# Optimization experiments

Measured on AMD Instinct MI355X. Metric: run time of the kernel, lower is better.

Reference implementation:

```python
import jax, jax.numpy as jnp
import numpy as np

LN_EPS = 1e-5  # torch nn.LayerNorm default


def layernorm(x, g, b):
    mu = jnp.mean(x, axis=-1, keepdims=True)
    var = jnp.var(x, axis=-1, keepdims=True)
    return (x - mu) * jax.lax.rsqrt(var + LN_EPS) * g + b


def setup_inputs() -> dict:
    key = jax.random.key(0)
    ks = jax.random.split(key, 12)
    B, N, Dn, Dm, E, L = 4, 20000, 64, 128, 160000, 2
    inp = {}
    inp["node_feat"] = jax.random.normal(ks[0], (B, N, Dn), jnp.float32)
    inp["in_W"] = jax.random.normal(ks[1], (Dn, Dm), jnp.float32) * 0.1
    inp["in_b"] = jnp.zeros((Dm,), jnp.float32)
    inp["node_W"] = jax.random.normal(ks[2], (L, 3, Dm, Dm), jnp.float32) * 0.05
    inp["node_b"] = jnp.zeros((L, 3, Dm), jnp.float32)
    inp["edge_W"] = jax.random.normal(ks[3], (L, 2, 16, Dm), jnp.float32) * 0.1
    inp["edge_b"] = jnp.zeros((L, 2, Dm), jnp.float32)
    inp["ln_g"] = jnp.ones((L, Dm), jnp.float32)
    inp["ln_b"] = jnp.zeros((L, Dm), jnp.float32)
    inp["ea0"] = jax.random.normal(ks[4], (E, 16), jnp.float32)
    inp["ea1"] = jax.random.normal(ks[5], (E, 16), jnp.float32)
    inp["ei0"] = jax.random.randint(ks[6], (2, E), 0, N)
    inp["ei1"] = jax.random.randint(ks[7], (2, E), 0, N)
    inp["ei2"] = jax.random.randint(ks[8], (2, E), 0, N)
    return inp


def reference(node_feat, in_W, in_b, node_W, node_b, edge_W, edge_b, ln_g, ln_b,
              ea0, ea1, ei0, ei1, ei2):
    # input projection: [B,N,Dn] -> [B,N,Dm]
    H = node_feat @ in_W + in_b
    edge_idx = [ei0, ei1, ei2]
    edge_attr = [ea0, ea1, None]  # relation 2 has edge_attr_dims == 0 (Identity/skip)
    n_layers = node_W.shape[0]
    for l in range(n_layers):
        agg = jnp.zeros_like(H)
        for r in range(3):
            src, dst = edge_idx[r][0], edge_idx[r][1]
            # gather src nodes per batch then per-relation linear: [B,E,Dm]
            msg = H[:, src] @ node_W[l, r] + node_b[l, r]
            if edge_attr[r] is not None:
                # edge attrs shared across batch -> broadcast add
                msg = msg + (edge_attr[r] @ edge_W[l, r] + edge_b[l, r])[None]
            # scatter-add messages to dst nodes, batched
            agg = agg.at[:, dst].add(msg)
        H = layernorm(H + jax.nn.relu(agg), ln_g[l], ln_b[l])
    return H
```

## Files before the change

kernel.cpp:

```cpp
#include <hip/hip_runtime.h>


#define NNODES 20000
#define NB     4
#define BROWS  (NB * NNODES)
#define DN     64
#define DM     128
#define NE     160000
#define CAP    64
#define LN_EPS 1e-5f
#define KE     448
#define LDW    88

typedef __attribute__((ext_vector_type(8))) short bf16x8;
typedef __attribute__((ext_vector_type(4))) float f32x4;

__device__ inline float bf2f(unsigned short u) {
    union { unsigned int i; float f; } x; x.i = ((unsigned int)u) << 16; return x.f;
}
__device__ inline unsigned short f2bf(float f) {
    union { float f; unsigned int i; } x; x.f = f;
    unsigned int r = x.i + 0x7FFFu + ((x.i >> 16) & 1u);
    return (unsigned short)(r >> 16);
}

__global__ void k_scatter(const int* __restrict__ ei0, const int* __restrict__ ei1,
                          const int* __restrict__ ei2, int* __restrict__ cursor,
                          int* __restrict__ srcs, int* __restrict__ eids) {
    int tid = blockIdx.x * blockDim.x + threadIdx.x;
    if (tid >= 3 * NE) return;
    int r = tid / NE, e = tid - r * NE;
    const int* ei = (r == 0) ? ei0 : ((r == 1) ? ei1 : ei2);
    int src = ei[e], dst = ei[NE + e];
    int p = atomicAdd(&cursor[r * NNODES + dst], 1);
    if (p < CAP) {
        srcs[(r * NNODES + dst) * CAP + p] = src;
        if (r < 2) eids[(r * NNODES + dst) * CAP + p] = e;
    }
}

__global__ __launch_bounds__(256) void k_sgather(const int* __restrict__ deg,
                                                 const int* __restrict__ eids,
                                                 const float* __restrict__ ea0,
                                                 const float* __restrict__ ea1,
                                                 float* __restrict__ S) {
    int task = blockIdx.x * 4 + (threadIdx.x >> 6);
    int r = task / NNODES;
    const float* ea = r ? ea1 : ea0;
    int lane = threadIdx.x & 63;
    int k = lane & 15, sub = lane >> 4;
    int dg = deg[task]; if (dg > CAP) dg = CAP;
    const int* bk = eids + (size_t)task * CAP;
    float acc = 0.f;
    for (int j = sub; j < dg; j += 4) {
        int e = bk[j];
        acc += ea[e * 16 + k];
    }
    acc += __shfl_xor(acc, 16, 64);
    acc += __shfl_xor(acc, 32, 64);
    if (lane < 16) S[(size_t)task * 16 + k] = acc;
}

__global__ __launch_bounds__(256) void k_wprep(const float* __restrict__ nW,
                                               const float* __restrict__ nb,
                                               const float* __restrict__ eW,
                                               const float* __restrict__ eb,
                                               const float* __restrict__ inW,
                                               unsigned short* __restrict__ Wt,
                                               unsigned short* __restrict__ Wp) {
    int lin = blockIdx.x * 256 + threadIdx.x;
    if (lin < 2 * 128 * KE) {
        int l = lin / (128 * KE);
        int rem = lin - l * 128 * KE;
        int n = rem / KE, k = rem - n * KE;
        float v;
        if (k < 384) {
            int r = k >> 7, kk = k & 127;
            v = nW[(((size_t)(l * 3 + r) * 128) + kk) * 128 + n];
        } else {
            int e = k - 384;
            if (e < 3) {
                v = nb[(l * 3 + e) * DM + n];
                if (e < 2) v += eb[(l * 2 + e) * DM + n];
            } else if (e < 35) {
                int r2 = (e - 3) >> 4, j = (e - 3) & 15;
                v = eW[((size_t)((l * 2 + r2) * 16 + j)) * DM + n];
            } else v = 0.f;
        }
        Wt[lin] = f2bf(v);
    } else {
        int i = lin - 2 * 128 * KE;
        int n = i >> 6, k = i & 63;
        Wp[n * 64 + k] = f2bf(inW[(size_t)k * DM + n]);
    }
}

__global__ __launch_bounds__(256) void k_proj(const float* __restrict__ X,
                                              const unsigned short* __restrict__ Wp,
                                              const float* __restrict__ bias,
                                              unsigned short* __restrict__ HB) {
    __shared__ __align__(16) unsigned short As[64][LDW];
    __shared__ __align__(16) unsigned short Bs[128][LDW];
    int t = threadIdx.x;
    int m0 = blockIdx.x * 64;
#pragma unroll
    for (int i = 0; i < 4; ++i) {
        int lin = t + 256 * i;
        int row = lin >> 4, seg = lin & 15;
        float4 v = *(const float4*)(X + (size_t)(m0 + row) * DN + seg * 4);
        ushort4 h; h.x = f2bf(v.x); h.y = f2bf(v.y); h.z = f2bf(v.z); h.w = f2bf(v.w);
        *(ushort4*)&As[row][seg * 4] = h;
    }
#pragma unroll
    for (int i = 0; i < 4; ++i) {
        int lin = t + 256 * i;
        int row = lin >> 3, seg = lin & 7;
        *(uint4*)&Bs[row][seg * 8] = *(const uint4*)(Wp + (size_t)row * 64 + seg * 8);
    }
    __syncthreads();
    int w = t >> 6, lane = t & 63;
    int q = lane >> 4, lm = lane & 15;
    f32x4 acc[8];
#pragma unroll
    for (int ct = 0; ct < 8; ++ct) acc[ct] = (f32x4){0.f, 0.f, 0.f, 0.f};
#pragma unroll
    for (int kt = 0; kt < 2; ++kt) {
        bf16x8 a = *(const bf16x8*)&As[w * 16 + lm][kt * 32 + q * 8];
#pragma unroll
        for (int ct = 0; ct < 8; ++ct) {
            bf16x8 bf = *(const bf16x8*)&Bs[ct * 16 + lm][kt * 32 + q * 8];
            acc[ct] = __builtin_amdgcn_mfma_f32_16x16x32_bf16(a, bf, acc[ct], 0, 0, 0);
        }
    }
#pragma unroll
    for (int reg = 0; reg < 4; ++reg) {
        int row = m0 + w * 16 + q * 4 + reg;
#pragma unroll
        for (int ct = 0; ct < 8; ++ct) {
            int col = ct * 16 + lm;
            HB[(size_t)row * DM + col] = f2bf(acc[ct][reg] + bias[col]);
        }
    }
}

__global__ __launch_bounds__(256) void k_spmm(const unsigned short* __restrict__ HB,
                                              const int* __restrict__ deg,
                                              const int* __restrict__ srcs,
                                              const float* __restrict__ S,
                                              unsigned short* __restrict__ G) {
    int blk = blockIdx.x;
    int s = blk & 7;
    int bb = s >> 1;
    int idx = ((blk >> 3) << 1) + (s & 1);
    int n0 = idx * 16;
    int g = threadIdx.x >> 4, lane = threadIdx.x & 15;
    int n = n0 + g;
    int c8 = lane * 8;
    const unsigned short* Hb = HB + (size_t)bb * NNODES * DM;
    size_t rowbase = ((size_t)(bb * NNODES + n)) * KE;
    int dt[3];
#pragma unroll
    for (int r = 0; r < 3; ++r) {
        dt[r] = deg[r * NNODES + n];
        int dg = dt[r] > CAP ? CAP : dt[r];
        const int* bk = srcs + (size_t)(r * NNODES + n) * CAP;
        float a[8];
#pragma unroll
        for (int j = 0; j < 8; ++j) a[j] = 0.f;
        int j = 0;
        for (; j + 3 < dg; j += 4) {
            int4 s4 = *(const int4*)&bk[j];
            ushort4 u0 = *(const ushort4*)(Hb + (size_t)s4.x * DM + c8);
            ushort4 u1 = *(const ushort4*)(Hb + (size_t)s4.x * DM + c8 + 4);
            ushort4 v0 = *(const ushort4*)(Hb + (size_t)s4.y * DM + c8);
            ushort4 v1 = *(const ushort4*)(Hb + (size_t)s4.y * DM + c8 + 4);
            ushort4 w0 = *(const ushort4*)(Hb + (size_t)s4.z * DM + c8);
            ushort4 w1 = *(const ushort4*)(Hb + (size_t)s4.z * DM + c8 + 4);
            ushort4 x0 = *(const ushort4*)(Hb + (size_t)s4.w * DM + c8);
            ushort4 x1 = *(const ushort4*)(Hb + (size_t)s4.w * DM + c8 + 4);
            a[0] += bf2f(u0.x) + bf2f(v0.x) + bf2f(w0.x) + bf2f(x0.x);
            a[1] += bf2f(u0.y) + bf2f(v0.y) + bf2f(w0.y) + bf2f(x0.y);
            a[2] += bf2f(u0.z) + bf2f(v0.z) + bf2f(w0.z) + bf2f(x0.z);
            a[3] += bf2f(u0.w) + bf2f(v0.w) + bf2f(w0.w) + bf2f(x0.w);
            a[4] += bf2f(u1.x) + bf2f(v1.x) + bf2f(w1.x) + bf2f(x1.x);
            a[5] += bf2f(u1.y) + bf2f(v1.y) + bf2f(w1.y) + bf2f(x1.y);
            a[6] += bf2f(u1.z) + bf2f(v1.z) + bf2f(w1.z) + bf2f(x1.z);
            a[7] += bf2f(u1.w) + bf2f(v1.w) + bf2f(w1.w) + bf2f(x1.w);
        }
        for (; j < dg; ++j) {
            int s0 = bk[j];
            ushort4 u0 = *(const ushort4*)(Hb + (size_t)s0 * DM + c8);
            ushort4 u1 = *(const ushort4*)(Hb + (size_t)s0 * DM + c8 + 4);
            a[0] += bf2f(u0.x); a[1] += bf2f(u0.y); a[2] += bf2f(u0.z); a[3] += bf2f(u0.w);
            a[4] += bf2f(u1.x); a[5] += bf2f(u1.y); a[6] += bf2f(u1.z); a[7] += bf2f(u1.w);
        }
        ushort4 o0, o1;
        o0.x = f2bf(a[0]); o0.y = f2bf(a[1]); o0.z = f2bf(a[2]); o0.w = f2bf(a[3]);
        o1.x = f2bf(a[4]); o1.y = f2bf(a[5]); o1.z = f2bf(a[6]); o1.w = f2bf(a[7]);
        *(ushort4*)(G + rowbase + r * 128 + c8) = o0;
        *(ushort4*)(G + rowbase + r * 128 + c8 + 4) = o1;
    }
    if (lane < 8) {
        ushort4 e0, e1;
        unsigned short ev[8];
#pragma unroll
        for (int j = 0; j < 8; ++j) {
            int kk = lane * 8 + j;
            float v;
            if (kk < 3)       v = (float)dt[kk];
            else if (kk < 19) v = S[((size_t)(0 * NNODES + n)) * 16 + (kk - 3)];
            else if (kk < 35) v = S[((size_t)(1 * NNODES + n)) * 16 + (kk - 19)];
            else              v = 0.f;
            ev[j] = f2bf(v);
        }
        e0.x = ev[0]; e0.y = ev[1]; e0.z = ev[2]; e0.w = ev[3];
        e1.x = ev[4]; e1.y = ev[5]; e1.z = ev[6]; e1.w = ev[7];
        *(ushort4*)(G + rowbase + 384 + lane * 8) = e0;
        *(ushort4*)(G + rowbase + 384 + lane * 8 + 4) = e1;
    }
}

__global__ __launch_bounds__(256) void k_gemm_ln(const unsigned short* __restrict__ G,
                                                 const unsigned short* __restrict__ Wt,
                                                 unsigned short* HB,
                                                 const float* __restrict__ lng,
                                                 const float* __restrict__ lnb,
                                                 float* __restrict__ out, int write_f32) {
    __shared__ __align__(16) unsigned short Gs[64][LDW];
    __shared__ __align__(16) unsigned short Ws[128][LDW];
    int t = threadIdx.x;
    int m0 = blockIdx.x * 64;
    int w = t >> 6, lane = t & 63;
    int q = lane >> 4, lm = lane & 15;

    f32x4 acc[8];
#pragma unroll
    for (int ct = 0; ct < 8; ++ct) acc[ct] = (f32x4){0.f, 0.f, 0.f, 0.f};

    for (int kc = 0; kc < 7; ++kc) {
#pragma unroll
        for (int i = 0; i < 2; ++i) {
            int lin = t + 256 * i;
            int row = lin >> 3, seg = lin & 7;
            *(uint4*)&Gs[row][seg * 8] =
                *(const uint4*)(G + (size_t)(m0 + row) * KE + kc * 64 + seg * 8);
        }
#pragma unroll
        for (int i = 0; i < 4; ++i) {
            int lin = t + 256 * i;
            int row = lin >> 3, seg = lin & 7;
            *(uint4*)&Ws[row][seg * 8] =
                *(const uint4*)(Wt + (size_t)row * KE + kc * 64 + seg * 8);
        }
        __syncthreads();
#pragma unroll
        for (int kt = 0; kt < 2; ++kt) {
            bf16x8 a = *(const bf16x8*)&Gs[w * 16 + lm][kt * 32 + q * 8];
#pragma unroll
            for (int ct = 0; ct < 8; ++ct) {
                bf16x8 bf = *(const bf16x8*)&Ws[ct * 16 + lm][kt * 32 + q * 8];
                acc[ct] = __builtin_amdgcn_mfma_f32_16x16x32_bf16(a, bf, acc[ct], 0, 0, 0);
            }
        }
        __syncthreads();
    }

    float gc[8], bc[8];
#pragma unroll
    for (int ct = 0; ct < 8; ++ct) {
        int col = ct * 16 + lm;
        gc[ct] = lng[col]; bc[ct] = lnb[col];
    }
#pragma unroll
    for (int reg = 0; reg < 4; ++reg) {
        size_t row = (size_t)m0 + w * 16 + q * 4 + reg;
        float xv[8];
        float s1 = 0.f, s2 = 0.f;
#pragma unroll
        for (int ct = 0; ct < 8; ++ct) {
            int col = ct * 16 + lm;
            float h = bf2f(HB[row * DM + col]);
            float v = h + fmaxf(acc[ct][reg], 0.f);
            xv[ct] = v; s1 += v; s2 += v * v;
        }
#pragma unroll
        for (int m = 1; m <= 8; m <<= 1) {
            s1 += __shfl_xor(s1, m, 64);
            s2 += __shfl_xor(s2, m, 64);
        }
        float mu  = s1 * (1.f / 128.f);
        float var = s2 * (1.f / 128.f) - mu * mu;
        float inv = rsqrtf(var + LN_EPS);
        if (write_f32) {
#pragma unroll
            for (int ct = 0; ct < 8; ++ct) {
                int col = ct * 16 + lm;
                out[row * DM + col] = (xv[ct] - mu) * inv * gc[ct] + bc[ct];
            }
        } else {
#pragma unroll
            for (int ct = 0; ct < 8; ++ct) {
                int col = ct * 16 + lm;
                HB[row * DM + col] = f2bf((xv[ct] - mu) * inv * gc[ct] + bc[ct]);
            }
        }
    }
}

extern "C" void kernel_launch(void* const* d_in, const int* in_sizes, int n_in,
                              void* d_out, int out_size, void* d_ws, size_t ws_size,
                              hipStream_t stream) {
    const float* node_feat = (const float*)d_in[0];
    const float* in_W   = (const float*)d_in[1];
    const float* in_b   = (const float*)d_in[2];
    const float* node_W = (const float*)d_in[3];
    const float* node_b = (const float*)d_in[4];
    const float* edge_W = (const float*)d_in[5];
    const float* edge_b = (const float*)d_in[6];
    const float* ln_g   = (const float*)d_in[7];
    const float* ln_b   = (const float*)d_in[8];
    const float* ea0    = (const float*)d_in[9];
    const float* ea1    = (const float*)d_in[10];
    const int*   ei0    = (const int*)d_in[11];
    const int*   ei1    = (const int*)d_in[12];
    const int*   ei2    = (const int*)d_in[13];
    float* out = (float*)d_out;

    char* ws = (char*)d_ws;
    size_t off = 0;
    auto alloc = [&](size_t bytes) -> void* {
        void* p = ws + off;
        off = (off + bytes + 255) & ~(size_t)255;
        return p;
    };
    unsigned short* HB     = (unsigned short*)alloc((size_t)BROWS * DM * 2);
    unsigned short* G      = (unsigned short*)alloc((size_t)BROWS * KE * 2);
    int*            cursor = (int*)alloc((size_t)3 * NNODES * 4);
    float*          S      = (float*)alloc((size_t)2 * NNODES * 16 * 4);
    int*            srcs   = (int*)alloc((size_t)3 * NNODES * CAP * 4);
    int*            eids   = (int*)alloc((size_t)2 * NNODES * CAP * 4);
    unsigned short* Wt     = (unsigned short*)alloc((size_t)2 * 128 * KE * 2);
    unsigned short* Wp     = (unsigned short*)alloc((size_t)128 * 64 * 2);

    hipMemsetAsync(cursor, 0, (size_t)3 * NNODES * 4, stream);

    k_scatter<<<(3 * NE + 255) / 256, 256, 0, stream>>>(ei0, ei1, ei2, cursor, srcs, eids);
    k_sgather<<<(2 * NNODES) / 4, 256, 0, stream>>>(cursor, eids, ea0, ea1, S);
    k_wprep<<<480, 256, 0, stream>>>(node_W, node_b, edge_W, edge_b, in_W, Wt, Wp);
    k_proj<<<BROWS / 64, 256, 0, stream>>>(node_feat, Wp, in_b, HB);

    for (int l = 0; l < 2; ++l) {
        k_spmm<<<5000, 256, 0, stream>>>(HB, cursor, srcs, S, G);
        k_gemm_ln<<<BROWS / 64, 256, 0, stream>>>(G, Wt + (size_t)l * 128 * KE, HB,
                                                  ln_g + (size_t)l * DM, ln_b + (size_t)l * DM,
                                                  out, l == 1);
    }
}
```

Measured before the change: 332.2 us.

## Prefetch gather indices, pre-scale source offsets, widen loads, double GEMM row tile

```diff
diff --git a/kernel.cpp b/kernel.cpp
--- a/kernel.cpp
+++ b/kernel.cpp
@@ -14,6 +14,8 @@
 
 typedef __attribute__((ext_vector_type(8))) short bf16x8;
 typedef __attribute__((ext_vector_type(4))) float f32x4;
+typedef __attribute__((ext_vector_type(2))) float f32x2;
+typedef __attribute__((ext_vector_type(8))) unsigned short u16x8;
 
 __device__ inline float bf2f(unsigned short u) {
     union { unsigned int i; float f; } x; x.i = ((unsigned int)u) << 16; return x.f;
@@ -22,6 +24,11 @@
     union { float f; unsigned int i; } x; x.f = f;
     unsigned int r = x.i + 0x7FFFu + ((x.i >> 16) & 1u);
     return (unsigned short)(r >> 16);
+}
+__device__ inline f32x2 bfpair(unsigned int w) {
+    union { unsigned int u; float f; } lo, hi;
+    lo.u = w << 16; hi.u = w & 0xffff0000u;
+    return (f32x2){lo.f, hi.f};
 }
 
 __global__ void k_scatter(const int* __restrict__ ei0, const int* __restrict__ ei1,
@@ -34,7 +41,7 @@
     int src = ei[e], dst = ei[NE + e];
     int p = atomicAdd(&cursor[r * NNODES + dst], 1);
     if (p < CAP) {
-        srcs[(r * NNODES + dst) * CAP + p] = src;
+        srcs[(r * NNODES + dst) * CAP + p] = src << 8;
         if (r < 2) eids[(r * NNODES + dst) * CAP + p] = e;
     }
 }
@@ -143,6 +150,34 @@
     }
 }
 
+__device__ inline void gather_rel(const char* __restrict__ HbB, unsigned c16,
+                                  const int* __restrict__ bk, int dg, int4 s4,
+                                  f32x2* a) {
+#pragma unroll
+    for (int i = 0; i < 4; ++i) a[i] = (f32x2){0.f, 0.f};
+    int j = 0;
+    while (j + 3 < dg) {
+        bool more = (j + 7 < dg);
+        int4 nxt = s4;
+        if (more) nxt = *(const int4*)(bk + j + 4);
+        uint4 u0 = *(const uint4*)(HbB + ((unsigned)s4.x + c16));
+        uint4 u1 = *(const uint4*)(HbB + ((unsigned)s4.y + c16));
+        uint4 u2 = *(const uint4*)(HbB + ((unsigned)s4.z + c16));
+        uint4 u3 = *(const uint4*)(HbB + ((unsigned)s4.w + c16));
+        a[0] += bfpair(u0.x) + bfpair(u1.x) + bfpair(u2.x) + bfpair(u3.x);
+        a[1] += bfpair(u0.y) + bfpair(u1.y) + bfpair(u2.y) + bfpair(u3.y);
+        a[2] += bfpair(u0.z) + bfpair(u1.z) + bfpair(u2.z) + bfpair(u3.z);
+        a[3] += bfpair(u0.w) + bfpair(u1.w) + bfpair(u2.w) + bfpair(u3.w);
+        j += 4;
+        s4 = nxt;
+    }
+    for (; j < dg; ++j) {
+        uint4 u = *(const uint4*)(HbB + ((unsigned)bk[j] + c16));
+        a[0] += bfpair(u.x); a[1] += bfpair(u.y);
+        a[2] += bfpair(u.z); a[3] += bfpair(u.w);
+    }
+}
+
 __global__ __launch_bounds__(256) void k_spmm(const unsigned short* __restrict__ HB,
                                               const int* __restrict__ deg,
                                               const int* __restrict__ srcs,
@@ -155,54 +190,39 @@
     int n0 = idx * 16;
     int g = threadIdx.x >> 4, lane = threadIdx.x & 15;
     int n = n0 + g;
-    int c8 = lane * 8;
-    const unsigned short* Hb = HB + (size_t)bb * NNODES * DM;
+    unsigned c16 = (unsigned)lane * 16;
+    const char* HbB = (const char*)HB + (size_t)bb * NNODES * DM * 2;
     size_t rowbase = ((size_t)(bb * NNODES + n)) * KE;
-    int dt[3];
-#pragma unroll
-    for (int r = 0; r < 3; ++r) {
-        dt[r] = deg[r * NNODES + n];
-        int dg = dt[r] > CAP ? CAP : dt[r];
-        const int* bk = srcs + (size_t)(r * NNODES + n) * CAP;
-        float a[8];
-#pragma unroll
-        for (int j = 0; j < 8; ++j) a[j] = 0.f;
-        int j = 0;
-        for (; j + 3 < dg; j += 4) {
-            int4 s4 = *(const int4*)&bk[j];
-            ushort4 u0 = *(const ushort4*)(Hb + (size_t)s4.x * DM + c8);
-            ushort4 u1 = *(const ushort4*)(Hb + (size_t)s4.x * DM + c8 + 4);
-            ushort4 v0 = *(const ushort4*)(Hb + (size_t)s4.y * DM + c8);
-            ushort4 v1 = *(const ushort4*)(Hb + (size_t)s4.y * DM + c8 + 4);
-            ushort4 w0 = *(const ushort4*)(Hb + (size_t)s4.z * DM + c8);
-            ushort4 w1 = *(const ushort4*)(Hb + (size_t)s4.z * DM + c8 + 4);
-            ushort4 x0 = *(const ushort4*)(Hb + (size_t)s4.w * DM + c8);
-            ushort4 x1 = *(const ushort4*)(Hb + (size_t)s4.w * DM + c8 + 4);
-            a[0] += bf2f(u0.x) + bf2f(v0.x) + bf2f(w0.x) + bf2f(x0.x);
-            a[1] += bf2f(u0.y) + bf2f(v0.y) + bf2f(w0.y) + bf2f(x0.y);
-            a[2] += bf2f(u0.z) + bf2f(v0.z) + bf2f(w0.z) + bf2f(x0.z);
-            a[3] += bf2f(u0.w) + bf2f(v0.w) + bf2f(w0.w) + bf2f(x0.w);
-            a[4] += bf2f(u1.x) + bf2f(v1.x) + bf2f(w1.x) + bf2f(x1.x);
-            a[5] += bf2f(u1.y) + bf2f(v1.y) + bf2f(w1.y) + bf2f(x1.y);
-            a[6] += bf2f(u1.z) + bf2f(v1.z) + bf2f(w1.z) + bf2f(x1.z);
-            a[7] += bf2f(u1.w) + bf2f(v1.w) + bf2f(w1.w) + bf2f(x1.w);
-        }
-        for (; j < dg; ++j) {
-            int s0 = bk[j];
-            ushort4 u0 = *(const ushort4*)(Hb + (size_t)s0 * DM + c8);
-            ushort4 u1 = *(const ushort4*)(Hb + (size_t)s0 * DM + c8 + 4);
-            a[0] += bf2f(u0.x); a[1] += bf2f(u0.y); a[2] += bf2f(u0.z); a[3] += bf2f(u0.w);
-            a[4] += bf2f(u1.x); a[5] += bf2f(u1.y); a[6] += bf2f(u1.z); a[7] += bf2f(u1.w);
-        }
-        ushort4 o0, o1;
-        o0.x = f2bf(a[0]); o0.y = f2bf(a[1]); o0.z = f2bf(a[2]); o0.w = f2bf(a[3]);
-        o1.x = f2bf(a[4]); o1.y = f2bf(a[5]); o1.z = f2bf(a[6]); o1.w = f2bf(a[7]);
-        *(ushort4*)(G + rowbase + r * 128 + c8) = o0;
-        *(ushort4*)(G + rowbase + r * 128 + c8 + 4) = o1;
-    }
+
+    int dt0 = deg[n], dt1 = deg[NNODES + n], dt2 = deg[2 * NNODES + n];
+    const int* bk0 = srcs + (size_t)n * CAP;
+    const int* bk1 = bk0 + (size_t)NNODES * CAP;
+    const int* bk2 = bk1 + (size_t)NNODES * CAP;
+    int4 f0 = *(const int4*)bk0;
+    int4 f1 = *(const int4*)bk1;
+    int4 f2 = *(const int4*)bk2;
+
+    f32x2 a[4];
+    u16x8 o;
+
+    gather_rel(HbB, c16, bk0, dt0 > CAP ? CAP : dt0, f0, a);
+#pragma unroll
+    for (int i = 0; i < 4; ++i) { o[2 * i] = f2bf(a[i].x); o[2 * i + 1] = f2bf(a[i].y); }
+    *(u16x8*)(G + rowbase + 0 * 128 + lane * 8) = o;
+
+    gather_rel(HbB, c16, bk1, dt1 > CAP ? CAP : dt1, f1, a);
+#pragma unroll
+    for (int i = 0; i < 4; ++i) { o[2 * i] = f2bf(a[i].x); o[2 * i + 1] = f2bf(a[i].y); }
+    *(u16x8*)(G + rowbase + 1 * 128 + lane * 8) = o;
+
+    gather_rel(HbB, c16, bk2, dt2 > CAP ? CAP : dt2, f2, a);
+#pragma unroll
+    for (int i = 0; i < 4; ++i) { o[2 * i] = f2bf(a[i].x); o[2 * i + 1] = f2bf(a[i].y); }
+    *(u16x8*)(G + rowbase + 2 * 128 + lane * 8) = o;
+
     if (lane < 8) {
-        ushort4 e0, e1;
-        unsigned short ev[8];
+        int dt[3] = {dt0, dt1, dt2};
+        u16x8 e;
 #pragma unroll
         for (int j = 0; j < 8; ++j) {
             int kk = lane * 8 + j;
@@ -211,12 +231,9 @@
             else if (kk < 19) v = S[((size_t)(0 * NNODES + n)) * 16 + (kk - 3)];
             else if (kk < 35) v = S[((size_t)(1 * NNODES + n)) * 16 + (kk - 19)];
             else              v = 0.f;
-            ev[j] = f2bf(v);
-        }
-        e0.x = ev[0]; e0.y = ev[1]; e0.z = ev[2]; e0.w = ev[3];
-        e1.x = ev[4]; e1.y = ev[5]; e1.z = ev[6]; e1.w = ev[7];
-        *(ushort4*)(G + rowbase + 384 + lane * 8) = e0;
-        *(ushort4*)(G + rowbase + 384 + lane * 8 + 4) = e1;
+            e[j] = f2bf(v);
+        }
+        *(u16x8*)(G + rowbase + 384 + lane * 8) = e;
     }
 }
 
@@ -226,20 +243,22 @@
                                                  const float* __restrict__ lng,
                                                  const float* __restrict__ lnb,
                                                  float* __restrict__ out, int write_f32) {
-    __shared__ __align__(16) unsigned short Gs[64][LDW];
+    __shared__ __align__(16) unsigned short Gs[128][LDW];
     __shared__ __align__(16) unsigned short Ws[128][LDW];
     int t = threadIdx.x;
-    int m0 = blockIdx.x * 64;
+    int m0 = blockIdx.x * 128;
     int w = t >> 6, lane = t & 63;
     int q = lane >> 4, lm = lane & 15;
 
-    f32x4 acc[8];
-#pragma unroll
-    for (int ct = 0; ct < 8; ++ct) acc[ct] = (f32x4){0.f, 0.f, 0.f, 0.f};
+    f32x4 acc[2][8];
+#pragma unroll
+    for (int af = 0; af < 2; ++af)
+#pragma unroll
+        for (int ct = 0; ct < 8; ++ct) acc[af][ct] = (f32x4){0.f, 0.f, 0.f, 0.f};
 
     for (int kc = 0; kc < 7; ++kc) {
 #pragma unroll
-        for (int i = 0; i < 2; ++i) {
+        for (int i = 0; i < 4; ++i) {
             int lin = t + 256 * i;
             int row = lin >> 3, seg = lin & 7;
             *(uint4*)&Gs[row][seg * 8] =
@@ -255,11 +274,13 @@
         __syncthreads();
 #pragma unroll
         for (int kt = 0; kt < 2; ++kt) {
-            bf16x8 a = *(const bf16x8*)&Gs[w * 16 + lm][kt * 32 + q * 8];
+            bf16x8 a0 = *(const bf16x8*)&Gs[w * 16 + lm][kt * 32 + q * 8];
+            bf16x8 a1 = *(const bf16x8*)&Gs[64 + w * 16 + lm][kt * 32 + q * 8];
 #pragma unroll
             for (int ct = 0; ct < 8; ++ct) {
                 bf16x8 bf = *(const bf16x8*)&Ws[ct * 16 + lm][kt * 32 + q * 8];
-                acc[ct] = __builtin_amdgcn_mfma_f32_16x16x32_bf16(a, bf, acc[ct], 0, 0, 0);
+                acc[0][ct] = __builtin_amdgcn_mfma_f32_16x16x32_bf16(a0, bf, acc[0][ct], 0, 0, 0);
+                acc[1][ct] = __builtin_amdgcn_mfma_f32_16x16x32_bf16(a1, bf, acc[1][ct], 0, 0, 0);
             }
         }
         __syncthreads();
@@ -272,36 +293,39 @@
         gc[ct] = lng[col]; bc[ct] = lnb[col];
     }
 #pragma unroll
-    for (int reg = 0; reg < 4; ++reg) {
-        size_t row = (size_t)m0 + w * 16 + q * 4 + reg;
-        float xv[8];
-        float s1 = 0.f, s2 = 0.f;
-#pragma unroll
-        for (int ct = 0; ct < 8; ++ct) {
-            int col = ct * 16 + lm;
-            float h = bf2f(HB[row * DM + col]);
-            float v = h + fmaxf(acc[ct][reg], 0.f);
-            xv[ct] = v; s1 += v; s2 += v * v;
-        }
-#pragma unroll
-        for (int m = 1; m <= 8; m <<= 1) {
-            s1 += __shfl_xor(s1, m, 64);
-            s2 += __shfl_xor(s2, m, 64);
-        }
-        float mu  = s1 * (1.f / 128.f);
-        float var = s2 * (1.f / 128.f) - mu * mu;
-        float inv = rsqrtf(var + LN_EPS);
-        if (write_f32) {
+    for (int af = 0; af < 2; ++af) {
+#pragma unroll
+        for (int reg = 0; reg < 4; ++reg) {
+            size_t row = (size_t)m0 + af * 64 + w * 16 + q * 4 + reg;
+            float xv[8];
+            float s1 = 0.f, s2 = 0.f;
 #pragma unroll
             for (int ct = 0; ct < 8; ++ct) {
                 int col = ct * 16 + lm;
-                out[row * DM + col] = (xv[ct] - mu) * inv * gc[ct] + bc[ct];
+                float h = bf2f(HB[row * DM + col]);
+                float v = h + fmaxf(acc[af][ct][reg], 0.f);
+                xv[ct] = v; s1 += v; s2 += v * v;
             }
-        } else {
-#pragma unroll
-            for (int ct = 0; ct < 8; ++ct) {
-                int col = ct * 16 + lm;
-                HB[row * DM + col] = f2bf((xv[ct] - mu) * inv * gc[ct] + bc[ct]);
+#pragma unroll
+            for (int m = 1; m <= 8; m <<= 1) {
+                s1 += __shfl_xor(s1, m, 64);
+                s2 += __shfl_xor(s2, m, 64);
+            }
+            float mu  = s1 * (1.f / 128.f);
+            float var = s2 * (1.f / 128.f) - mu * mu;
+            float inv = rsqrtf(var + LN_EPS);
+            if (write_f32) {
+#pragma unroll
+                for (int ct = 0; ct < 8; ++ct) {
+                    int col = ct * 16 + lm;
+                    out[row * DM + col] = (xv[ct] - mu) * inv * gc[ct] + bc[ct];
+                }
+            } else {
+#pragma unroll
+                for (int ct = 0; ct < 8; ++ct) {
+                    int col = ct * 16 + lm;
+                    HB[row * DM + col] = f2bf((xv[ct] - mu) * inv * gc[ct] + bc[ct]);
+                }
             }
         }
     }
@@ -351,8 +375,8 @@
 
     for (int l = 0; l < 2; ++l) {
         k_spmm<<<5000, 256, 0, stream>>>(HB, cursor, srcs, S, G);
-        k_gemm_ln<<<BROWS / 64, 256, 0, stream>>>(G, Wt + (size_t)l * 128 * KE, HB,
-                                                  ln_g + (size_t)l * DM, ln_b + (size_t)l * DM,
-                                                  out, l == 1);
-    }
-}
+        k_gemm_ln<<<BROWS / 128, 256, 0, stream>>>(G, Wt + (size_t)l * 128 * KE, HB,
+                                                   ln_g + (size_t)l * DM, ln_b + (size_t)l * DM,
+                                                   out, l == 1);
+    }
+}
```

Result: slower. 344.8 us (+3.8%).
